# Optimization experiments

Hardware: AMD Instinct MI355X
Metric: run time of the kernel (lower is better)

## Reference

```python
import jax, jax.numpy as jnp
import numpy as np

N_NODES = 100000
N_EDGES = 1600000
IN_DIM, HID_DIM, OUT_DIM = 128, 128, 64


def setup_inputs() -> dict:
    key = jax.random.key(0)
    k1, k2, k3, k4 = jax.random.split(key, 4)
    x = jax.random.normal(k1, (N_NODES, IN_DIM), dtype=jnp.float32)
    edge_index = jax.random.randint(k2, (2, N_EDGES), 0, N_NODES, dtype=jnp.int64)
    # Glorot-ish init for weights, zeros for biases (as in PyG GCNConv defaults)
    W1 = jax.random.normal(k3, (IN_DIM, HID_DIM), dtype=jnp.float32) * (1.0 / np.sqrt(IN_DIM))
    b1 = jnp.zeros((HID_DIM,), dtype=jnp.float32)
    W2 = jax.random.normal(k4, (HID_DIM, OUT_DIM), dtype=jnp.float32) * (1.0 / np.sqrt(HID_DIM))
    b2 = jnp.zeros((OUT_DIM,), dtype=jnp.float32)
    return {"x": x, "edge_index": edge_index, "W1": W1, "b1": b1, "W2": W2, "b2": b2}


def _build_norm(edge_index, num_nodes):
    """Add self-loops and compute symmetric GCN normalization per edge.
    Returns (src, dst, norm) with self-loops appended."""
    loops = jnp.arange(num_nodes, dtype=edge_index.dtype)
    src = jnp.concatenate([edge_index[0], loops])
    dst = jnpp_concat = jnp.concatenate([edge_index[1], loops])
    deg = jax.ops.segment_sum(jnp.ones_like(dst, dtype=jnp.float32), dst,
                              num_segments=num_nodes)
    dinv = jax.lax.rsqrt(deg)  # deg >= 1 due to self-loops
    norm = dinv[src] * dinv[dst]  # [E + N]
    return src, dst, norm


def _gcn_conv(h, W, b, src, dst, norm, num_nodes):
    h = h @ W                                   # [N, F_out]
    msg = h[src] * norm[:, None]                # gather + scale, [E+N, F_out]
    agg = jax.ops.segment_sum(msg, dst, num_segments=num_nodes)
    return agg + b


def reference(x, edge_index, W1, b1, W2, b2):
    num_nodes = x.shape[0]
    src, dst, norm = _build_norm(edge_index, num_nodes)
    h = jax.nn.relu(_gcn_conv(x, W1, b1, src, dst, norm, num_nodes))
    return _gcn_conv(h, W2, b2, src, dst, norm, num_nodes)
```

## Files before the change

kernel.cpp:

```cpp
#include <hip/hip_runtime.h>

#define NN 100000
#define NE 1600000
#define NB 782
#define NBPAD 1024
#define CAPB 3072
#define EPB 8192
#define NROWPAD 100096
#define DPAD 136
#define OPAD 72

typedef __attribute__((ext_vector_type(8))) short short8;
typedef __attribute__((ext_vector_type(4))) float f32x4;

__device__ __forceinline__ unsigned short bf16rn(float f) {
    unsigned u = __float_as_uint(f);
    return (unsigned short)((u + 0x7FFFu + ((u >> 16) & 1u)) >> 16);
}
__device__ __forceinline__ float4 bf2x4(uint2 g) {
    float4 r;
    r.x = __uint_as_float(g.x << 16);
    r.y = __uint_as_float(g.x & 0xFFFF0000u);
    r.z = __uint_as_float(g.y << 16);
    r.w = __uint_as_float(g.y & 0xFFFF0000u);
    return r;
}
__device__ __forceinline__ uint2 packbf4(float4 v) {
    uint2 u;
    u.x = (unsigned)bf16rn(v.x) | ((unsigned)bf16rn(v.y) << 16);
    u.y = (unsigned)bf16rn(v.z) | ((unsigned)bf16rn(v.w) << 16);
    return u;
}
__device__ __forceinline__ void acc4(float4& a, uint2 v, unsigned qb) {
    float q = __uint_as_float(qb);
    a.x = fmaf(__uint_as_float(v.x << 16), q, a.x);
    a.y = fmaf(__uint_as_float(v.x & 0xFFFF0000u), q, a.y);
    a.z = fmaf(__uint_as_float(v.y << 16), q, a.z);
    a.w = fmaf(__uint_as_float(v.y & 0xFFFF0000u), q, a.w);
}

__global__ void detect_i64_k(const unsigned* __restrict__ ei, int* __restrict__ flag) {
    unsigned w = ei[2 * threadIdx.x + 1];
    unsigned long long b = __ballot(w == 0u);
    if (threadIdx.x == 0) *flag = (b == 0xFFFFFFFFFFFFFFFFull) ? 1 : 0;
}
__device__ __forceinline__ int load_node(const void* ei, int i64, long long idx) {
    return i64 ? (int)((const long long*)ei)[idx] : ((const int*)ei)[idx];
}

__global__ void cast_bf16_k(const float* __restrict__ in, ushort* __restrict__ outb,
                            long long n4) {
    long long i = (long long)blockIdx.x * 256 + threadIdx.x;
    if (i >= n4) return;
    ((uint2*)outb)[i] = packbf4(((const float4*)in)[i]);
}

__global__ void prep_wt_k(const float* __restrict__ W1, const float* __restrict__ W2,
                          ushort* __restrict__ W1t, ushort* __restrict__ W2t) {
    int i = blockIdx.x * 256 + threadIdx.x;
    if (i < 128 * 128) {
        int k = i >> 7, n = i & 127;
        W1t[n * 128 + k] = bf16rn(W1[k * 128 + n]);
    }
    if (i < 128 * 64) {
        int k = i >> 6, n = i & 63;
        W2t[n * 128 + k] = bf16rn(W2[k * 64 + n]);
    }
}

__global__ __launch_bounds__(256) void binfill_k(const void* __restrict__ ei,
                                                 const int* __restrict__ flag,
                                                 int* __restrict__ cur,
                                                 unsigned* __restrict__ bstage) {
    __shared__ unsigned binned[EPB];
    __shared__ int lcnt[NBPAD];
    __shared__ int lpos[NBPAD];
    __shared__ int gbase[NBPAD];
    __shared__ int tsum[256];
    int tid = threadIdx.x;
    long long e0 = (long long)blockIdx.x * EPB;
    int i64 = *flag;

    for (int i = tid; i < NBPAD; i += 256) lcnt[i] = 0;
    __syncthreads();

    for (int i = tid; i < EPB; i += 256) {
        long long e = e0 + i;
        if (e < NE) {
            int d = load_node(ei, i64, (long long)NE + e);
            atomicAdd(&lcnt[d >> 7], 1);
        }
    }
    __syncthreads();

    int base = tid * 4;
    int c0 = lcnt[base], c1 = lcnt[base + 1], c2 = lcnt[base + 2], c3 = lcnt[base + 3];
    int s = c0 + c1 + c2 + c3;
    tsum[tid] = s;
    __syncthreads();
    for (int off = 1; off < 256; off <<= 1) {
        int v = (tid >= off) ? tsum[tid - off] : 0;
        __syncthreads();
        tsum[tid] += v;
        __syncthreads();
    }
    int excl = tsum[tid] - s;
    int p0 = excl, p1 = excl + c0, p2 = p1 + c1, p3 = p2 + c2;
    lcnt[base] = p0; lcnt[base + 1] = p1; lcnt[base + 2] = p2; lcnt[base + 3] = p3;
    lpos[base] = p0; lpos[base + 1] = p1; lpos[base + 2] = p2; lpos[base + 3] = p3;
    if (base < NB)     gbase[base]     = c0 ? atomicAdd(&cur[base], c0) : 0;
    if (base + 1 < NB) gbase[base + 1] = c1 ? atomicAdd(&cur[base + 1], c1) : 0;
    if (base + 2 < NB) gbase[base + 2] = c2 ? atomicAdd(&cur[base + 2], c2) : 0;
    if (base + 3 < NB) gbase[base + 3] = c3 ? atomicAdd(&cur[base + 3], c3) : 0;
    __syncthreads();

    for (int i = tid; i < EPB; i += 256) {
        long long e = e0 + i;
        if (e < NE) {
            int sv = load_node(ei, i64, e);
            int d  = load_node(ei, i64, (long long)NE + e);
            int b  = d >> 7;
            int p  = atomicAdd(&lpos[b], 1);
            binned[p] = ((unsigned)(d & 127) << 17) | (unsigned)sv;
        }
    }
    __syncthreads();

    for (int b = tid; b < NB; b += 256) {
        int start = lcnt[b], endp = lpos[b];
        int gb = gbase[b];
        unsigned* dst = bstage + (long long)b * CAPB;
        for (int k = start; k < endp; k++) {
            int go = gb + (k - start);
            if (go < CAPB) dst[go] = binned[k];
        }
    }
}

__global__ __launch_bounds__(256) void regroup_k(const int* __restrict__ cur,
                                                 const unsigned* __restrict__ bstage,
                                                 int* __restrict__ cnt,
                                                 int* __restrict__ rowstart,
                                                 uint2* __restrict__ g2,
                                                 float* __restrict__ dinv) {
    __shared__ unsigned stash[CAPB];
    __shared__ int lcnt[128], lofs[128], lpos[128], sc[128];
    int tid = threadIdx.x;
    int b = blockIdx.x;

    int total = cur[b];
    if (total > CAPB) total = CAPB;
    const unsigned* seg = bstage + (long long)b * CAPB;
    for (int i = tid; i < total; i += 256) stash[i] = seg[i];
    __syncthreads();

    if (tid < 128) { lcnt[tid] = 0; lpos[tid] = 0; }
    __syncthreads();
    for (int i = tid; i < total; i += 256)
        atomicAdd(&lcnt[stash[i] >> 17], 1);
    __syncthreads();

    if (tid < 128) sc[tid] = lcnt[tid];
    __syncthreads();
    for (int off = 1; off < 128; off <<= 1) {
        int v = 0;
        if (tid < 128 && tid >= off) v = sc[tid - off];
        __syncthreads();
        if (tid < 128) sc[tid] += v;
        __syncthreads();
    }
    if (tid < 128) {
        lofs[tid] = sc[tid] - lcnt[tid];
        int node = b * 128 + tid;
        if (node < NN) {
            cnt[node] = lcnt[tid];
            rowstart[node] = b * CAPB + lofs[tid];
            dinv[node] = rsqrtf((float)(lcnt[tid] + 1));
        }
    }
    __syncthreads();

    uint2* g = g2 + (long long)b * CAPB;
    for (int i = tid; i < total; i += 256) {
        unsigned e = stash[i];
        int nl = e >> 17;
        int p = atomicAdd(&lpos[nl], 1);
        g[lofs[nl] + p] = make_uint2(e & 0x1FFFFu, (unsigned)(b * 128 + nl));
    }
}

__global__ __launch_bounds__(256) void qn_k(const int* __restrict__ cur,
                                            const float* __restrict__ dinv,
                                            uint2* __restrict__ g2) {
    int b = blockIdx.x;
    int total = cur[b];
    if (total > CAPB) total = CAPB;
    uint2* g = g2 + (long long)b * CAPB;
    for (int i = threadIdx.x; i < total; i += 256) {
        uint2 e = g[i];
        float q = dinv[e.x] * dinv[e.y];
        g[i] = make_uint2(e.x, __float_as_uint(q));
    }
}

template <int LPN, bool BIAS, bool OUTB>
__global__ __launch_bounds__(256) void pull3_k(const uint2* __restrict__ g2,
                                               const int* __restrict__ rowstart,
                                               const int* __restrict__ cnt,
                                               const float* __restrict__ dinv,
                                               const ushort* __restrict__ hb,
                                               const float* __restrict__ bias,
                                               void* __restrict__ out) {
    int tid = threadIdx.x;
    int node = blockIdx.x * (256 / LPN) + tid / LPN;
    int lane = tid & (LPN - 1);
    if (node >= NN) return;

    const uint2* h2 = (const uint2*)hb;
    float di = dinv[node];
    float w0 = di * di;
    float4 A = make_float4(0.f, 0.f, 0.f, 0.f);
    float4 B = make_float4(0.f, 0.f, 0.f, 0.f);
    {
        float4 hv = bf2x4(h2[(unsigned)node * LPN + lane]);
        A.x = hv.x * w0; A.y = hv.y * w0; A.z = hv.z * w0; A.w = hv.w * w0;
    }

    int deg = cnt[node];
    const uint2* row = g2 + rowstart[node];

    int j = 0;
    if (deg >= 4) {
        uint2 e0 = row[0], e1 = row[1], e2 = row[2], e3 = row[3];
        uint2 v0 = h2[e0.x * LPN + lane];
        uint2 v1 = h2[e1.x * LPN + lane];
        uint2 v2 = h2[e2.x * LPN + lane];
        uint2 v3 = h2[e3.x * LPN + lane];
        for (; j + 8 <= deg; j += 4) {
            uint2 f0 = row[j + 4], f1 = row[j + 5], f2 = row[j + 6], f3 = row[j + 7];
            acc4(A, v0, e0.y); acc4(B, v1, e1.y);
            acc4(A, v2, e2.y); acc4(B, v3, e3.y);
            uint2 w0v = h2[f0.x * LPN + lane];
            uint2 w1v = h2[f1.x * LPN + lane];
            uint2 w2v = h2[f2.x * LPN + lane];
            uint2 w3v = h2[f3.x * LPN + lane];
            e0 = f0; e1 = f1; e2 = f2; e3 = f3;
            v0 = w0v; v1 = w1v; v2 = w2v; v3 = w3v;
        }
        acc4(A, v0, e0.y); acc4(B, v1, e1.y);
        acc4(A, v2, e2.y); acc4(B, v3, e3.y);
        j += 4;
    }
    for (; j < deg; j++) {
        uint2 e = row[j];
        uint2 v = h2[e.x * LPN + lane];
        acc4(A, v, e.y);
    }

    float4 o;
    o.x = A.x + B.x; o.y = A.y + B.y; o.z = A.z + B.z; o.w = A.w + B.w;
    if (BIAS) {
        float4 bb = ((const float4*)bias)[lane];
        o.x += bb.x; o.y += bb.y; o.z += bb.z; o.w += bb.w;
    }
    if (OUTB)
        ((uint2*)out)[(unsigned)node * LPN + lane] = packbf4(o);
    else
        ((float4*)out)[(unsigned)node * LPN + lane] = o;
}

__global__ __launch_bounds__(256) void dgemm_mfma_k(const ushort* __restrict__ Ab,
                                                    const ushort* __restrict__ W1t,
                                                    const float* __restrict__ b1,
                                                    const ushort* __restrict__ W2t,
                                                    ushort* __restrict__ H2b) {
    __shared__ ushort Tt[4][32 * DPAD];
    __shared__ ushort Ot[4][32 * OPAD];
    int tid = threadIdx.x;
    int wv = tid >> 6, lane = tid & 63;
    int m16 = lane & 15, quad = lane >> 4;
    int row0 = blockIdx.x * 128 + wv * 32;

    short8 af[2][4];
#pragma unroll
    for (int mt = 0; mt < 2; mt++)
#pragma unroll
        for (int kc = 0; kc < 4; kc++)
            af[mt][kc] = *(const short8*)(Ab + (long long)(row0 + mt * 16 + m16) * 128
                                          + kc * 32 + quad * 8);
    f32x4 accA[2][8];
#pragma unroll
    for (int mt = 0; mt < 2; mt++)
#pragma unroll
        for (int nt = 0; nt < 8; nt++) accA[mt][nt] = (f32x4){0.f, 0.f, 0.f, 0.f};

#pragma unroll
    for (int nt = 0; nt < 8; nt++) {
#pragma unroll
        for (int kc = 0; kc < 4; kc++) {
            short8 bf = *(const short8*)(W1t + (nt * 16 + m16) * 128 + kc * 32 + quad * 8);
            accA[0][nt] = __builtin_amdgcn_mfma_f32_16x16x32_bf16(af[0][kc], bf, accA[0][nt], 0, 0, 0);
            accA[1][nt] = __builtin_amdgcn_mfma_f32_16x16x32_bf16(af[1][kc], bf, accA[1][nt], 0, 0, 0);
        }
    }

#pragma unroll
    for (int nt = 0; nt < 8; nt++) {
        float bb = b1[nt * 16 + m16];
#pragma unroll
        for (int mt = 0; mt < 2; mt++)
#pragma unroll
            for (int r = 0; r < 4; r++) {
                float v = fmaxf(accA[mt][nt][r] + bb, 0.f);
                Tt[wv][(mt * 16 + quad * 4 + r) * DPAD + nt * 16 + m16] = bf16rn(v);
            }
    }
    __syncthreads();

    f32x4 accB[2][4];
#pragma unroll
    for (int mt = 0; mt < 2; mt++)
#pragma unroll
        for (int nt = 0; nt < 4; nt++) accB[mt][nt] = (f32x4){0.f, 0.f, 0.f, 0.f};

#pragma unroll
    for (int nt = 0; nt < 4; nt++) {
#pragma unroll
        for (int kc = 0; kc < 4; kc++) {
            short8 bf = *(const short8*)(W2t + (nt * 16 + m16) * 128 + kc * 32 + quad * 8);
#pragma unroll
            for (int mt = 0; mt < 2; mt++) {
                short8 aT = *(const short8*)(&Tt[wv][(mt * 16 + m16) * DPAD + kc * 32 + quad * 8]);
                accB[mt][nt] = __builtin_amdgcn_mfma_f32_16x16x32_bf16(aT, bf, accB[mt][nt], 0, 0, 0);
            }
        }
    }

#pragma unroll
    for (int nt = 0; nt < 4; nt++)
#pragma unroll
        for (int mt = 0; mt < 2; mt++)
#pragma unroll
            for (int r = 0; r < 4; r++)
                Ot[wv][(mt * 16 + quad * 4 + r) * OPAD + nt * 16 + m16] = bf16rn(accB[mt][nt][r]);
    __syncthreads();

    uint4* H4 = (uint4*)H2b;
#pragma unroll
    for (int it = 0; it < 4; it++) {
        int idx = it * 64 + lane;
        int r = idx >> 3, c = idx & 7;
        int grow = row0 + r;
        if (grow < NN) {
            uint4 v = *(const uint4*)(&Ot[wv][r * OPAD + c * 8]);
            H4[(long long)grow * 8 + c] = v;
        }
    }
}

extern "C" void kernel_launch(void* const* d_in, const int* in_sizes, int n_in,
                              void* d_out, int out_size, void* d_ws, size_t ws_size,
                              hipStream_t stream) {
    const float* x  = (const float*)d_in[0];
    const void*  ei = d_in[1];
    const float* W1 = (const float*)d_in[2];
    const float* b1 = (const float*)d_in[3];
    const float* W2 = (const float*)d_in[4];
    const float* b2 = (const float*)d_in[5];
    float* out = (float*)d_out;
    char* ws = (char*)d_ws;

    int*      flag     = (int*)ws;
    int*      cur      = (int*)(ws + 0x1000);
    int*      cnt      = (int*)(ws + 0x10000);
    int*      rowstart = (int*)(ws + 0x80000);
    unsigned* bstage   = (unsigned*)(ws + 0x100000);
    uint2*    g2       = (uint2*)(ws + 0xB00000);
    ushort*   xb       = (ushort*)(ws + 0x1E00000);
    ushort*   aggxb    = (ushort*)(ws + 0x3700000);
    ushort*   h2b      = (ushort*)(ws + 0x5000000);
    ushort*   W1t      = (ushort*)(ws + 0x5D00000);
    ushort*   W2t      = (ushort*)(ws + 0x5D10000);
    float*    dinv     = (float*)(ws + 0x5D20000);

    hipMemsetAsync(cur, 0, NB * sizeof(int), stream);
    detect_i64_k<<<1, 64, 0, stream>>>((const unsigned*)ei, flag);
    cast_bf16_k<<<(NN * 32 + 255) / 256, 256, 0, stream>>>(x, xb, (long long)NN * 32);
    prep_wt_k<<<64, 256, 0, stream>>>(W1, W2, W1t, W2t);
    binfill_k<<<(NE + EPB - 1) / EPB, 256, 0, stream>>>(ei, flag, cur, bstage);
    regroup_k<<<NB, 256, 0, stream>>>(cur, bstage, cnt, rowstart, g2, dinv);
    qn_k<<<NB, 256, 0, stream>>>(cur, dinv, g2);

    pull3_k<32, false, true><<<(NN + 7) / 8, 256, 0, stream>>>(g2, rowstart, cnt, dinv,
                                                               xb, nullptr, aggxb);
    dgemm_mfma_k<<<NROWPAD / 128, 256, 0, stream>>>(aggxb, W1t, b1, W2t, h2b);

    pull3_k<16, true, false><<<(NN + 15) / 16, 256, 0, stream>>>(g2, rowstart, cnt, dinv,
                                                                 h2b, b2, out);
}
```

Before: 325.7 us.

## Stage edge lists in LDS, deepen gather prefetch, and swizzle blocks across XCDs

The neighbor-pull aggregation kernel now has the lanes of each node cooperatively copy up to 64 edge entries into shared memory. It then runs the feature gather with an 8-deep register prefetch pipeline instead of 4-deep. Block indices are remapped so that contiguous node ranges land on the same XCD, which should improve L2 locality for row and output accesses. The aim is more memory-level parallelism on the random h-row gathers and less redundant global reading of edge records. The cost is extra LDS use and register pressure. Correctness depends on the LDS writes and reads for a node staying within one wavefront, since there is no explicit barrier.

```diff
diff --git a/kernel.cpp b/kernel.cpp
--- a/kernel.cpp
+++ b/kernel.cpp
@@ -9,6 +9,7 @@
 #define NROWPAD 100096
 #define DPAD 136
 #define OPAD 72
+#define MAXE 64
 
 typedef __attribute__((ext_vector_type(8))) short short8;
 typedef __attribute__((ext_vector_type(4))) float f32x4;
@@ -37,6 +38,12 @@
     a.y = fmaf(__uint_as_float(v.x & 0xFFFF0000u), q, a.y);
     a.z = fmaf(__uint_as_float(v.y << 16), q, a.z);
     a.w = fmaf(__uint_as_float(v.y & 0xFFFF0000u), q, a.w);
+}
+__device__ __forceinline__ int xcd_swz(int bid, int nwg) {
+    int q = nwg >> 3, r = nwg & 7;
+    int x = bid & 7, j = bid >> 3;
+    int base = (x < r) ? x * (q + 1) : r * (q + 1) + (x - r) * q;
+    return base + j;
 }
 
 __global__ void detect_i64_k(const unsigned* __restrict__ ei, int* __restrict__ flag) {
@@ -204,16 +211,18 @@
 }
 
 template <int LPN, bool BIAS, bool OUTB>
-__global__ __launch_bounds__(256) void pull3_k(const uint2* __restrict__ g2,
+__global__ __launch_bounds__(256) void pull4_k(const uint2* __restrict__ g2,
                                                const int* __restrict__ rowstart,
                                                const int* __restrict__ cnt,
                                                const float* __restrict__ dinv,
                                                const ushort* __restrict__ hb,
                                                const float* __restrict__ bias,
                                                void* __restrict__ out) {
+    __shared__ uint2 ed[256 / LPN][MAXE];
     int tid = threadIdx.x;
-    int node = blockIdx.x * (256 / LPN) + tid / LPN;
+    int nib = tid / LPN;
     int lane = tid & (LPN - 1);
+    int node = xcd_swz(blockIdx.x, (int)gridDim.x) * (256 / LPN) + nib;
     if (node >= NN) return;
 
     const uint2* h2 = (const uint2*)hb;
@@ -228,33 +237,46 @@
 
     int deg = cnt[node];
     const uint2* row = g2 + rowstart[node];
+    int s = deg < MAXE ? deg : MAXE;
+
+    for (int t = lane; t < s; t += LPN) ed[nib][t] = row[t];
 
     int j = 0;
-    if (deg >= 4) {
-        uint2 e0 = row[0], e1 = row[1], e2 = row[2], e3 = row[3];
-        uint2 v0 = h2[e0.x * LPN + lane];
-        uint2 v1 = h2[e1.x * LPN + lane];
-        uint2 v2 = h2[e2.x * LPN + lane];
-        uint2 v3 = h2[e3.x * LPN + lane];
-        for (; j + 8 <= deg; j += 4) {
-            uint2 f0 = row[j + 4], f1 = row[j + 5], f2 = row[j + 6], f3 = row[j + 7];
-            acc4(A, v0, e0.y); acc4(B, v1, e1.y);
-            acc4(A, v2, e2.y); acc4(B, v3, e3.y);
-            uint2 w0v = h2[f0.x * LPN + lane];
-            uint2 w1v = h2[f1.x * LPN + lane];
-            uint2 w2v = h2[f2.x * LPN + lane];
-            uint2 w3v = h2[f3.x * LPN + lane];
-            e0 = f0; e1 = f1; e2 = f2; e3 = f3;
-            v0 = w0v; v1 = w1v; v2 = w2v; v3 = w3v;
-        }
-        acc4(A, v0, e0.y); acc4(B, v1, e1.y);
-        acc4(A, v2, e2.y); acc4(B, v3, e3.y);
-        j += 4;
+    if (s >= 8) {
+        uint2 v[8];
+        unsigned q[8];
+#pragma unroll
+        for (int t = 0; t < 8; t++) {
+            uint2 e = ed[nib][t];
+            q[t] = e.y;
+            v[t] = h2[e.x * LPN + lane];
+        }
+        for (; j + 16 <= s; j += 8) {
+#pragma unroll
+            for (int t = 0; t < 8; t++) {
+                uint2 e = ed[nib][j + 8 + t];
+                uint2 nv = h2[e.x * LPN + lane];
+                if (t & 1) acc4(B, v[t], q[t]);
+                else       acc4(A, v[t], q[t]);
+                v[t] = nv; q[t] = e.y;
+            }
+        }
+#pragma unroll
+        for (int t = 0; t < 8; t++) {
+            if (t & 1) acc4(B, v[t], q[t]);
+            else       acc4(A, v[t], q[t]);
+        }
+        j += 8;
+    }
+    for (; j < s; j++) {
+        uint2 e = ed[nib][j];
+        uint2 v0 = h2[e.x * LPN + lane];
+        acc4(A, v0, e.y);
     }
     for (; j < deg; j++) {
         uint2 e = row[j];
-        uint2 v = h2[e.x * LPN + lane];
-        acc4(A, v, e.y);
+        uint2 v0 = h2[e.x * LPN + lane];
+        acc4(A, v0, e.y);
     }
 
     float4 o;
@@ -391,10 +413,10 @@
     regroup_k<<<NB, 256, 0, stream>>>(cur, bstage, cnt, rowstart, g2, dinv);
     qn_k<<<NB, 256, 0, stream>>>(cur, dinv, g2);
 
-    pull3_k<32, false, true><<<(NN + 7) / 8, 256, 0, stream>>>(g2, rowstart, cnt, dinv,
+    pull4_k<32, false, true><<<(NN + 7) / 8, 256, 0, stream>>>(g2, rowstart, cnt, dinv,
                                                                xb, nullptr, aggxb);
     dgemm_mfma_k<<<NROWPAD / 128, 256, 0, stream>>>(aggxb, W1t, b1, W2t, h2b);
 
-    pull3_k<16, true, false><<<(NN + 15) / 16, 256, 0, stream>>>(g2, rowstart, cnt, dinv,
+    pull4_k<16, true, false><<<(NN + 15) / 16, 256, 0, stream>>>(g2, rowstart, cnt, dinv,
                                                                  h2b, b2, out);
 }
```

New measurement: 317.8 us. -2.4%, faster.
